# Kernel tuning notes

Hardware: AMD Instinct MI355X
Metric: run time of the kernel (lower is better)

## Reference

```python
import jax, jax.numpy as jnp
import numpy as np

N_NODES = 50000
N_EDGES = 800000
IN_C, HID_C, OUT_C = 128, 256, 64


def _linear_params(key, fan_in, fan_out):
    kw, kb = jax.random.split(key)
    bound = 1.0 / np.sqrt(fan_in)
    w = jax.random.uniform(kw, (fan_in, fan_out), jnp.float32, -bound, bound)
    b = jax.random.uniform(kb, (fan_out,), jnp.float32, -bound, bound)
    return w, b


def setup_inputs() -> dict:
    key = jax.random.key(0)
    ks = jax.random.split(key, 8)
    x = jax.random.normal(ks[0], (N_NODES, IN_C), jnp.float32)
    edge_index = jax.random.randint(ks[1], (2, N_EDGES), 0, N_NODES, dtype=jnp.int64)
    w1a, b1a = _linear_params(ks[2], IN_C, HID_C)
    w1b, b1b = _linear_params(ks[3], HID_C, HID_C)
    w2a, b2a = _linear_params(ks[4], HID_C, HID_C)
    w2b, b2b = _linear_params(ks[5], HID_C, HID_C)
    w3a, b3a = _linear_params(ks[6], HID_C, HID_C)
    w3b, b3b = _linear_params(ks[7], HID_C, OUT_C)
    return {
        "x": x, "edge_index": edge_index,
        "w1a": w1a, "b1a": b1a, "w1b": w1b, "b1b": b1b,
        "w2a": w2a, "b2a": b2a, "w2b": w2b, "b2b": b2b,
        "w3a": w3a, "b3a": b3a, "w3b": w3b, "b3b": b3b,
    }


def _gin_conv(x, src, dst, wa, ba, wb, bb):
    # GINConv (eps=0): MLP( x + sum_{j->i} x_j )
    agg = jax.ops.segment_sum(x[src], dst, num_segments=N_NODES)  # [N, d]
    h = x + agg
    h = jnp.maximum(h @ wa + ba, 0.0)
    return h @ wb + bb


def reference(x, edge_index, w1a, b1a, w1b, b1b, w2a, b2a, w2b, b2b,
              w3a, b3a, w3b, b3b):
    src, dst = edge_index[0], edge_index[1]
    h = jnp.maximum(_gin_conv(x, src, dst, w1a, b1a, w1b, b1b), 0.0)
    h = jnp.maximum(_gin_conv(h, src, dst, w2a, b2a, w2b, b2b), 0.0)
    # output head: Linear -> ReLU -> Dropout(eval: identity) -> Linear
    h = jnp.maximum(h @ w3a + b3a, 0.0)
    return h @ w3b + b3b  # [N, OUT_C]
```

## Files before the change

### kernel.cpp

```cpp
#include <hip/hip_runtime.h>
#include <stdint.h>

#define N_NODES 50000
#define N_EDGES 800000
#define M_PAD   50048
#define NREP    4
#define MCAP    8
#define SCAP    24
#define BCAP    (MCAP + SCAP)
#define CSTR    50048
#define NPX     6256
#define TSTR    264

typedef __attribute__((ext_vector_type(8))) short bf16x8;
typedef __attribute__((ext_vector_type(4))) float f32x4;

__device__ __forceinline__ unsigned short f2b(float f){
    unsigned int u = __builtin_bit_cast(unsigned int, f);
    u += 0x7fffu + ((u >> 16) & 1u);
    return (unsigned short)(u >> 16);
}
__device__ __forceinline__ float b2f(unsigned short s){
    unsigned int u = ((unsigned int)s) << 16;
    return __builtin_bit_cast(float, u);
}

__device__ __forceinline__ void gl_lds16(const void* g, void* l){
    __builtin_amdgcn_global_load_lds(
        (const __attribute__((address_space(1))) void*)g,
        (__attribute__((address_space(3))) void*)l, 16, 0, 0);
}

__global__ void k_x2b(const float* __restrict__ x, unsigned short* __restrict__ xs,
                      int* __restrict__ cnt){
    int gi = blockIdx.x * 256 + threadIdx.x;
    if (gi < NREP * CSTR) cnt[gi] = 0;
    size_t e0 = (size_t)gi * 8;
    if (e0 >= (size_t)M_PAD * 128) return;
    int node = (int)(e0 >> 7);
    int ch0  = (int)(e0 & 127);
    int sl = ch0 >> 5, wth = ch0 & 31;
    bf16x8 o;
    if (node < N_NODES){
        const float4* xp = (const float4*)(x + e0);
        float4 a = xp[0], b = xp[1];
        o[0] = (short)f2b(a.x); o[1] = (short)f2b(a.y);
        o[2] = (short)f2b(a.z); o[3] = (short)f2b(a.w);
        o[4] = (short)f2b(b.x); o[5] = (short)f2b(b.y);
        o[6] = (short)f2b(b.z); o[7] = (short)f2b(b.w);
    } else {
#pragma unroll
        for (int i = 0; i < 8; ++i) o[i] = 0;
    }
    *(bf16x8*)&xs[((size_t)(sl * 50048 + node)) * 32 + wth] = o;
}

__global__ __launch_bounds__(256) void k_scatter(const int* __restrict__ ei,
        int* __restrict__ cnt, unsigned short* __restrict__ mn,
        unsigned short* __restrict__ sp){
    const int x = blockIdx.x & 7;
    const int c = blockIdx.x >> 3;
    const int nlo = x * NPX, nhi = nlo + NPX;
    const int r = threadIdx.x & 3;
#pragma unroll
    for (int i = 0; i < 4; ++i){
        int e = c * 1024 + i * 256 + threadIdx.x;
        if (e < N_EDGES){
            int d = ei[N_EDGES + e];
            if (d >= nlo && d < nhi && (unsigned)d < N_NODES){
                unsigned s = (unsigned)ei[e];
                if (s < N_NODES){
                    int p = atomicAdd(&cnt[r * CSTR + d], 1);
                    int b = (d << 2) + r;
                    if (p < MCAP) mn[(b << 3) + p] = (unsigned short)s;
                    else if (p < BCAP) sp[b * SCAP + (p - MCAP)] = (unsigned short)s;
                }
            }
        }
    }
}

__global__ void k_scan1(const int* __restrict__ cnt, int* __restrict__ bsum){
    __shared__ int s[256];
    int t = threadIdx.x, n = blockIdx.x * 256 + t;
    int v = 0;
    if (n < M_PAD){
#pragma unroll
        for (int r = 0; r < 4; ++r){
            int c = cnt[r * CSTR + n];
            v += (c > BCAP) ? BCAP : c;
        }
        v = (v + 3) & ~3;
    }
    s[t] = v;
    __syncthreads();
    for (int off = 128; off > 0; off >>= 1){
        if (t < off) s[t] += s[t + off];
        __syncthreads();
    }
    if (t == 0) bsum[blockIdx.x] = s[0];
}

__global__ void k_scan2(const int* __restrict__ bsum, int* __restrict__ boff){
    __shared__ int s[256];
    int t = threadIdx.x;
    int v = (t < 196) ? bsum[t] : 0;
    s[t] = v;
    __syncthreads();
    for (int off = 1; off < 256; off <<= 1){
        int a = (t >= off) ? s[t - off] : 0;
        __syncthreads();
        s[t] += a;
        __syncthreads();
    }
    boff[t] = s[t] - v;
}

__global__ void k_scan3(const int* __restrict__ cnt, const int* __restrict__ boff,
                        int* __restrict__ mgoff){
    __shared__ int s[256];
    int t = threadIdx.x, n = blockIdx.x * 256 + t;
    int v = 0;
    if (n < M_PAD){
#pragma unroll
        for (int r = 0; r < 4; ++r){
            int c = cnt[r * CSTR + n];
            v += (c > BCAP) ? BCAP : c;
        }
        v = (v + 3) & ~3;
    }
    s[t] = v;
    __syncthreads();
    for (int off = 1; off < 256; off <<= 1){
        int a = (t >= off) ? s[t - off] : 0;
        __syncthreads();
        s[t] += a;
        __syncthreads();
    }
    if (n < M_PAD) mgoff[n] = boff[blockIdx.x] + s[t] - v;
}

__global__ void k_merge(const int* __restrict__ cnt, const int* __restrict__ mgoff,
                        const unsigned short* __restrict__ mn, const unsigned short* __restrict__ sp,
                        unsigned short* __restrict__ mg, int* __restrict__ mginfo){
    const int t = threadIdx.x;
    const int r = t & 3;
    const int n = blockIdx.x * 64 + (t >> 2);
    int c = cnt[r * CSTR + n];
    if (c > BCAP) c = BCAP;
    int incl = c;
    int t1 = __shfl_up(incl, 1, 4); if (r >= 1) incl += t1;
    int t2 = __shfl_up(incl, 2, 4); if (r >= 2) incl += t2;
    const int excl = incl - c;
    const int total = __shfl(incl, 3, 4);
    const unsigned mb = (unsigned)mgoff[n];
    const unsigned short* src = &mn[((n << 2) + r) << 3];
    for (int i = 0; i < c && i < MCAP; ++i)
        mg[mb + excl + i] = src[i];
    const unsigned short* ssrc = &sp[((n << 2) + r) * SCAP];
    for (int i = MCAP; i < c; ++i)
        mg[mb + excl + i] = ssrc[i - MCAP];
    if (r == 3){
        int grp = (total + 3) >> 2;
        mginfo[n] = ((int)mb << 6) | grp;
        for (int pos = total; pos < grp * 4; ++pos) mg[mb + pos] = (unsigned short)N_NODES;
    }
}

template<int C, bool SPLIT>
__global__ __launch_bounds__(256) void k_aggx(const unsigned short* __restrict__ in,
        const int* __restrict__ mginfo, const unsigned short* __restrict__ mg,
        unsigned short* __restrict__ out){
    constexpr int RS = C / 8;
    const int bid = blockIdx.x, w8 = bid & 7;
    int g, nbase;
    if (SPLIT){ g = w8 & 3; nbase = ((bid >> 3) + (w8 >> 2) * 391) * 64; }
    else      { g = w8;     nbase = (bid >> 3) * 64; }
    const int lane = threadIdx.x & 63, wid = threadIdx.x >> 6;
    const int qd = lane >> 2, lq = lane & 3;
    const int n = nbase + wid * 16 + qd;
    const bf16x8* __restrict__ xr = (const bf16x8*)in;
    const unsigned sbu = (unsigned)g * 50048u;

    float a[8];
    {
        bf16x8 s = xr[(sbu + (unsigned)n) * 4u + (unsigned)lq];
#pragma unroll
        for (int i = 0; i < 8; ++i) a[i] = b2f((unsigned short)s[i]);
    }
    const int info = mginfo[n];
    const int grp = info & 63;
    const unsigned mbase = (unsigned)(info >> 6);
    for (int k = 0; k < grp; ++k){
        ushort4 jj = *(const ushort4*)&mg[mbase + (unsigned)(k * 4)];
        bf16x8 v0 = xr[(sbu + jj.x) * 4u + lq];
        bf16x8 v1 = xr[(sbu + jj.y) * 4u + lq];
        bf16x8 v2 = xr[(sbu + jj.z) * 4u + lq];
        bf16x8 v3 = xr[(sbu + jj.w) * 4u + lq];
#pragma unroll
        for (int i = 0; i < 8; ++i)
            a[i] += (b2f((unsigned short)v0[i]) + b2f((unsigned short)v1[i]))
                  + (b2f((unsigned short)v2[i]) + b2f((unsigned short)v3[i]));
    }
    bf16x8 o;
#pragma unroll
    for (int i = 0; i < 8; ++i) o[i] = (short)f2b(a[i]);
    *(bf16x8*)&out[((unsigned)n * RS + (unsigned)(g * 4 + lq)) * 8u] = o;
}

__global__ void k_wt_all(const float* w0, const float* w1, const float* w2,
                         const float* w3, const float* w4, const float* w5,
                         unsigned short* o0, unsigned short* o1, unsigned short* o2,
                         unsigned short* o3, unsigned short* o4, unsigned short* o5){
    const int Ks[6]  = {128, 256, 256, 256, 256, 256};
    const int Ns[6]  = {256, 256, 256, 256, 256,  64};
    const int NPs[6] = {256, 256, 256, 256, 256, 128};
    int s = blockIdx.y;
    const float* w = (s == 0) ? w0 : (s == 1) ? w1 : (s == 2) ? w2
                   : (s == 3) ? w3 : (s == 4) ? w4 : w5;
    unsigned short* o = (s == 0) ? o0 : (s == 1) ? o1 : (s == 2) ? o2
                      : (s == 3) ? o3 : (s == 4) ? o4 : o5;
    int K = Ks[s], N = Ns[s], NP = NPs[s];
    int idx = blockIdx.x * 256 + threadIdx.x;
    if (idx >= NP * K) return;
    int np = idx / K, k = idx - np * K;
    float v = (np < N) ? w[(size_t)k * N + np] : 0.f;
    o[idx] = f2b(v);
}

template<int K1, int NMID, int NOUT, bool RELU_OUT, bool BF16OUT, bool SLICED>
__global__ __launch_bounds__(256) void k_mlp2(const unsigned short* __restrict__ A,
        const unsigned short* __restrict__ WA, const float* __restrict__ bA,
        const unsigned short* __restrict__ WB, const float* __restrict__ bB,
        void* __restrict__ out, int mstore){
    constexpr int NFA = NMID / 32;
    constexpr int NFB = NOUT / 32;
    __shared__ alignas(16) unsigned short As[64 * 32];
    __shared__ alignas(16) unsigned short Bs[NMID * 32];
    __shared__ alignas(16) unsigned short T[64 * TSTR];
    const int tid  = threadIdx.x;
    const int lane = tid & 63;
    const int c = lane & 15, qq = lane >> 4;
    const int kk = qq * 8;
    const int row0 = blockIdx.x * 64;
    const int wm = (tid >> 6) >> 1, wn = (tid >> 6) & 1;

    const f32x4 fzero = {0.f, 0.f, 0.f, 0.f};
    const char* Ab = (const char*)A;

    {
        f32x4 acc[NFA][2];
#pragma unroll
        for (int nf = 0; nf < NFA; ++nf){ acc[nf][0] = fzero; acc[nf][1] = fzero; }
        const char* Wb = (const char*)WA;
        for (int kt = 0; kt < K1 / 32; ++kt){
            {
                const int o = tid * 16;
                gl_lds16(Ab + ((size_t)(row0 + (o >> 6)) * K1 + kt * 32) * 2 + (o & 63),
                         (char*)As + o);
            }
#pragma unroll
            for (int ch = 0; ch < NMID / 64; ++ch){
                const int o = ch * 4096 + tid * 16;
                gl_lds16(Wb + ((size_t)(o >> 6) * K1 + kt * 32) * 2 + (o & 63),
                         (char*)Bs + o);
            }
            __syncthreads();
            bf16x8 xf[2];
#pragma unroll
            for (int mf = 0; mf < 2; ++mf)
                xf[mf] = *(const bf16x8*)&As[(wm * 32 + mf * 16 + c) * 32 + kk];
#pragma unroll
            for (int nf = 0; nf < NFA; ++nf){
                bf16x8 wf = *(const bf16x8*)&Bs[((wn * NFA + nf) * 16 + c) * 32 + kk];
#pragma unroll
                for (int mf = 0; mf < 2; ++mf)
                    acc[nf][mf] = __builtin_amdgcn_mfma_f32_16x16x32_bf16(wf, xf[mf], acc[nf][mf], 0, 0, 0);
            }
            __syncthreads();
        }
#pragma unroll
        for (int nf = 0; nf < NFA; ++nf){
            const int nb = wn * (NFA * 16) + nf * 16 + qq * 4;
            const float4 bb = *(const float4*)&bA[nb];
#pragma unroll
            for (int mf = 0; mf < 2; ++mf){
                const int ml = wm * 32 + mf * 16 + c;
                float v0 = fmaxf(acc[nf][mf][0] + bb.x, 0.f);
                float v1 = fmaxf(acc[nf][mf][1] + bb.y, 0.f);
                float v2 = fmaxf(acc[nf][mf][2] + bb.z, 0.f);
                float v3 = fmaxf(acc[nf][mf][3] + bb.w, 0.f);
                uint2 p;
                p.x = (unsigned)f2b(v0) | ((unsigned)f2b(v1) << 16);
                p.y = (unsigned)f2b(v2) | ((unsigned)f2b(v3) << 16);
                *(uint2*)&T[ml * TSTR + nb] = p;
            }
        }
    }
    __syncthreads();

    {
        f32x4 acc[NFB][2];
#pragma unroll
        for (int nf = 0; nf < NFB; ++nf){ acc[nf][0] = fzero; acc[nf][1] = fzero; }
        const char* Wb = (const char*)WB;
        for (int kt = 0; kt < NMID / 32; ++kt){
#pragma unroll
            for (int ch = 0; ch < NOUT / 64; ++ch){
                const int o = ch * 4096 + tid * 16;
                gl_lds16(Wb + ((size_t)(o >> 6) * NMID + kt * 32) * 2 + (o & 63),
                         (char*)Bs + o);
            }
            __syncthreads();
            bf16x8 xf[2];
#pragma unroll
            for (int mf = 0; mf < 2; ++mf)
                xf[mf] = *(const bf16x8*)&T[(wm * 32 + mf * 16 + c) * TSTR + kt * 32 + kk];
#pragma unroll
            for (int nf = 0; nf < NFB; ++nf){
                bf16x8 wf = *(const bf16x8*)&Bs[((wn * NFB + nf) * 16 + c) * 32 + kk];
#pragma unroll
                for (int mf = 0; mf < 2; ++mf)
                    acc[nf][mf] = __builtin_amdgcn_mfma_f32_16x16x32_bf16(wf, xf[mf], acc[nf][mf], 0, 0, 0);
            }
            __syncthreads();
        }
#pragma unroll
        for (int nf = 0; nf < NFB; ++nf){
            const int nb = wn * (NFB * 16) + nf * 16 + qq * 4;
            const float4 bb = *(const float4*)&bB[nb];
#pragma unroll
            for (int mf = 0; mf < 2; ++mf){
                const int m = row0 + wm * 32 + mf * 16 + c;
                if (m < mstore){
                    float v0 = acc[nf][mf][0] + bb.x;
                    float v1 = acc[nf][mf][1] + bb.y;
                    float v2 = acc[nf][mf][2] + bb.z;
                    float v3 = acc[nf][mf][3] + bb.w;
                    if (RELU_OUT){
                        v0 = fmaxf(v0, 0.f); v1 = fmaxf(v1, 0.f);
                        v2 = fmaxf(v2, 0.f); v3 = fmaxf(v3, 0.f);
                    }
                    if (SLICED){
                        uint2 p;
                        p.x = (unsigned)f2b(v0) | ((unsigned)f2b(v1) << 16);
                        p.y = (unsigned)f2b(v2) | ((unsigned)f2b(v3) << 16);
                        if (m >= N_NODES){ p.x = 0; p.y = 0; }
                        *(uint2*)&((unsigned short*)out)[
                            ((size_t)((nb >> 5) * 50048 + m)) * 32 + (nb & 31)] = p;
                    } else if (BF16OUT){
                        uint2 p;
                        p.x = (unsigned)f2b(v0) | ((unsigned)f2b(v1) << 16);
                        p.y = (unsigned)f2b(v2) | ((unsigned)f2b(v3) << 16);
                        *(uint2*)&((unsigned short*)out)[(size_t)m * NOUT + nb] = p;
                    } else {
                        float4 p = make_float4(v0, v1, v2, v3);
                        *(float4*)&((float*)out)[(size_t)m * NOUT + nb] = p;
                    }
                }
            }
        }
    }
}

extern "C" void kernel_launch(void* const* d_in, const int* in_sizes, int n_in,
                              void* d_out, int out_size, void* d_ws, size_t ws_size,
                              hipStream_t stream){
    const float* x   = (const float*)d_in[0];
    const int*   ei  = (const int*)d_in[1];
    const float* w1a = (const float*)d_in[2];
    const float* b1a = (const float*)d_in[3];
    const float* w1b = (const float*)d_in[4];
    const float* b1b = (const float*)d_in[5];
    const float* w2a = (const float*)d_in[6];
    const float* b2a = (const float*)d_in[7];
    const float* w2b = (const float*)d_in[8];
    const float* b2b = (const float*)d_in[9];
    const float* w3a = (const float*)d_in[10];
    const float* b3a = (const float*)d_in[11];
    const float* w3b = (const float*)d_in[12];
    const float* b3b = (const float*)d_in[13];

    char* ws = (char*)d_ws;
    size_t off = 0;
    auto take = [&](size_t bytes) -> char* {
        off = (off + 255) & ~(size_t)255;
        char* p = ws + off;
        off += bytes;
        return p;
    };
    unsigned short* xs1  = (unsigned short*)take((size_t)4 * 50048 * 32 * 2);
    unsigned short* g1   = (unsigned short*)take((size_t)M_PAD * 128 * 2);
    unsigned short* h1s  = (unsigned short*)take((size_t)8 * 50048 * 32 * 2);
    unsigned short* g2   = (unsigned short*)take((size_t)M_PAD * 256 * 2);
    unsigned short* h2   = (unsigned short*)take((size_t)M_PAD * 256 * 2);
    unsigned short* wt1a = (unsigned short*)take(256 * 128 * 2);
    unsigned short* wt1b = (unsigned short*)take(256 * 256 * 2);
    unsigned short* wt2a = (unsigned short*)take(256 * 256 * 2);
    unsigned short* wt2b = (unsigned short*)take(256 * 256 * 2);
    unsigned short* wt3a = (unsigned short*)take(256 * 256 * 2);
    unsigned short* wt3b = (unsigned short*)take(128 * 256 * 2);
    int*            cnt  = (int*)take((size_t)NREP * CSTR * 4);
    unsigned short* mn   = (unsigned short*)take((size_t)M_PAD * 4 * MCAP * 2);
    unsigned short* sp   = (unsigned short*)take((size_t)M_PAD * 4 * SCAP * 2);
    unsigned short* mg   = (unsigned short*)take((size_t)1100000 * 2);
    int*            mgoff  = (int*)take((size_t)M_PAD * 4);
    int*            mginfo = (int*)take((size_t)M_PAD * 4);
    int*            bsum = (int*)take(256 * 4);
    int*            boff = (int*)take(256 * 4);

    k_x2b<<<(M_PAD * 128 / 8 + 255) / 256, 256, 0, stream>>>(x, xs1, cnt);
    k_scatter<<<782 * 8, 256, 0, stream>>>(ei, cnt, mn, sp);
    k_scan1<<<196, 256, 0, stream>>>(cnt, bsum);
    k_scan2<<<1,   256, 0, stream>>>(bsum, boff);
    k_scan3<<<196, 256, 0, stream>>>(cnt, boff, mgoff);
    k_merge<<<782, 256, 0, stream>>>(cnt, mgoff, mn, sp, mg, mginfo);
    k_wt_all<<<dim3(256, 6), 256, 0, stream>>>(w1a, w1b, w2a, w2b, w3a, w3b,
                                               wt1a, wt1b, wt2a, wt2b, wt3a, wt3b);

    k_aggx<128, true ><<<391 * 8, 256, 0, stream>>>(xs1, mginfo, mg, g1);
    k_mlp2<128, 256, 256, true, true, true><<<M_PAD / 64, 256, 0, stream>>>(
        g1, wt1a, b1a, wt1b, b1b, h1s, M_PAD);
    k_aggx<256, false><<<782 * 8, 256, 0, stream>>>(h1s, mginfo, mg, g2);
    k_mlp2<256, 256, 256, true, true, false><<<M_PAD / 64, 256, 0, stream>>>(
        g2, wt2a, b2a, wt2b, b2b, h2, M_PAD);
    k_mlp2<256, 256, 64, false, false, false><<<M_PAD / 64, 256, 0, stream>>>(
        h2, wt3a, b3a, wt3b, b3b, d_out, N_NODES);
}
```

Before: 217.9 us.

## Sort nodes by degree bucket for aggregation and sort neighbor lists

Adds a degree histogram and counting sort that builds a node permutation grouping nodes of equal padded degree, so each aggregation wavefront processes nodes with similar neighbor counts and suffers less loop divergence. The scan kernels are restructured to compute the histogram and the per-bin offsets. The merge step now insertion-sorts each replica's neighbor list by source index, which should give more local gather addresses. In exchange it adds an extra indirection through perm, atomics in the scans, and per-thread sorting in merge. Output rows still land at their original node index.

```diff
diff --git a/kernel.cpp b/kernel.cpp
--- a/kernel.cpp
+++ b/kernel.cpp
@@ -10,6 +10,7 @@
 #define BCAP    (MCAP + SCAP)
 #define CSTR    50048
 #define NPX     6256
+#define BINS    33
 #define TSTR    264
 
 typedef __attribute__((ext_vector_type(8))) short bf16x8;
@@ -31,10 +32,21 @@
         (__attribute__((address_space(3))) void*)l, 16, 0, 0);
 }
 
+__device__ __forceinline__ int pdeg(const int* __restrict__ cnt, int n){
+    int v = 0;
+#pragma unroll
+    for (int r = 0; r < 4; ++r){
+        int c = cnt[r * CSTR + n];
+        v += (c > BCAP) ? BCAP : c;
+    }
+    return (v + 3) & ~3;
+}
+
 __global__ void k_x2b(const float* __restrict__ x, unsigned short* __restrict__ xs,
-                      int* __restrict__ cnt){
+                      int* __restrict__ cnt, int* __restrict__ ghist){
     int gi = blockIdx.x * 256 + threadIdx.x;
     if (gi < NREP * CSTR) cnt[gi] = 0;
+    if (gi < BINS) ghist[gi] = 0;
     size_t e0 = (size_t)gi * 8;
     if (e0 >= (size_t)M_PAD * 128) return;
     int node = (int)(e0 >> 7);
@@ -80,28 +92,27 @@
     }
 }
 
-__global__ void k_scan1(const int* __restrict__ cnt, int* __restrict__ bsum){
+__global__ void k_scanA(const int* __restrict__ cnt, int* __restrict__ bsum,
+                        int* __restrict__ ghist){
     __shared__ int s[256];
+    __shared__ int h[BINS];
     int t = threadIdx.x, n = blockIdx.x * 256 + t;
-    int v = 0;
-    if (n < M_PAD){
-#pragma unroll
-        for (int r = 0; r < 4; ++r){
-            int c = cnt[r * CSTR + n];
-            v += (c > BCAP) ? BCAP : c;
-        }
-        v = (v + 3) & ~3;
-    }
+    if (t < BINS) h[t] = 0;
+    int v = (n < M_PAD) ? pdeg(cnt, n) : 0;
     s[t] = v;
+    __syncthreads();
+    if (n < M_PAD) atomicAdd(&h[v >> 2], 1);
     __syncthreads();
     for (int off = 128; off > 0; off >>= 1){
         if (t < off) s[t] += s[t + off];
         __syncthreads();
     }
     if (t == 0) bsum[blockIdx.x] = s[0];
-}
-
-__global__ void k_scan2(const int* __restrict__ bsum, int* __restrict__ boff){
+    if (t < BINS && h[t] > 0) atomicAdd(&ghist[t], h[t]);
+}
+
+__global__ void k_scanB(const int* __restrict__ bsum, int* __restrict__ boff,
+                        const int* __restrict__ ghist, int* __restrict__ bincur){
     __shared__ int s[256];
     int t = threadIdx.x;
     int v = (t < 196) ? bsum[t] : 0;
@@ -113,23 +124,10 @@
         s[t] += a;
         __syncthreads();
     }
-    boff[t] = s[t] - v;
-}
-
-__global__ void k_scan3(const int* __restrict__ cnt, const int* __restrict__ boff,
-                        int* __restrict__ mgoff){
-    __shared__ int s[256];
-    int t = threadIdx.x, n = blockIdx.x * 256 + t;
-    int v = 0;
-    if (n < M_PAD){
-#pragma unroll
-        for (int r = 0; r < 4; ++r){
-            int c = cnt[r * CSTR + n];
-            v += (c > BCAP) ? BCAP : c;
-        }
-        v = (v + 3) & ~3;
-    }
-    s[t] = v;
+    if (t < 196) boff[t] = s[t] - v;
+    __syncthreads();
+    int w = (t < BINS) ? ghist[t] : 0;
+    s[t] = w;
     __syncthreads();
     for (int off = 1; off < 256; off <<= 1){
         int a = (t >= off) ? s[t - off] : 0;
@@ -137,7 +135,35 @@
         s[t] += a;
         __syncthreads();
     }
-    if (n < M_PAD) mgoff[n] = boff[blockIdx.x] + s[t] - v;
+    if (t < BINS) bincur[t] = s[t] - w;
+}
+
+__global__ void k_scanC(const int* __restrict__ cnt, const int* __restrict__ boff,
+                        int* __restrict__ mgoff, int* __restrict__ bincur,
+                        unsigned short* __restrict__ perm){
+    __shared__ int s[256];
+    __shared__ int h[BINS];
+    __shared__ int hb[BINS];
+    int t = threadIdx.x, n = blockIdx.x * 256 + t;
+    int v = (n < M_PAD) ? pdeg(cnt, n) : 0;
+    int grp = v >> 2;
+    s[t] = v;
+    if (t < BINS) h[t] = 0;
+    __syncthreads();
+    int lpos = 0;
+    if (n < M_PAD) lpos = atomicAdd(&h[grp], 1);
+    __syncthreads();
+    if (t < BINS && h[t] > 0) hb[t] = atomicAdd(&bincur[t], h[t]);
+    for (int off = 1; off < 256; off <<= 1){
+        int a = (t >= off) ? s[t - off] : 0;
+        __syncthreads();
+        s[t] += a;
+        __syncthreads();
+    }
+    if (n < M_PAD){
+        mgoff[n] = boff[blockIdx.x] + s[t] - v;
+        perm[hb[grp] + lpos] = (unsigned short)n;
+    }
 }
 
 __global__ void k_merge(const int* __restrict__ cnt, const int* __restrict__ mgoff,
@@ -148,18 +174,25 @@
     const int n = blockIdx.x * 64 + (t >> 2);
     int c = cnt[r * CSTR + n];
     if (c > BCAP) c = BCAP;
+    unsigned short v[BCAP];
+    const unsigned short* src = &mn[((n << 2) + r) << 3];
+    for (int i = 0; i < c && i < MCAP; ++i) v[i] = src[i];
+    const unsigned short* ssrc = &sp[((n << 2) + r) * SCAP];
+    for (int i = MCAP; i < c; ++i) v[i] = ssrc[i - MCAP];
+    for (int i = 1; i < c; ++i){
+        unsigned short key = v[i];
+        int j = i - 1;
+        while (j >= 0 && v[j] > key){ v[j + 1] = v[j]; --j; }
+        v[j + 1] = key;
+    }
     int incl = c;
     int t1 = __shfl_up(incl, 1, 4); if (r >= 1) incl += t1;
     int t2 = __shfl_up(incl, 2, 4); if (r >= 2) incl += t2;
     const int excl = incl - c;
     const int total = __shfl(incl, 3, 4);
     const unsigned mb = (unsigned)mgoff[n];
-    const unsigned short* src = &mn[((n << 2) + r) << 3];
-    for (int i = 0; i < c && i < MCAP; ++i)
-        mg[mb + excl + i] = src[i];
-    const unsigned short* ssrc = &sp[((n << 2) + r) * SCAP];
-    for (int i = MCAP; i < c; ++i)
-        mg[mb + excl + i] = ssrc[i - MCAP];
+    for (int i = 0; i < c; ++i)
+        mg[mb + excl + i] = v[i];
     if (r == 3){
         int grp = (total + 3) >> 2;
         mginfo[n] = ((int)mb << 6) | grp;
@@ -170,15 +203,15 @@
 template<int C, bool SPLIT>
 __global__ __launch_bounds__(256) void k_aggx(const unsigned short* __restrict__ in,
         const int* __restrict__ mginfo, const unsigned short* __restrict__ mg,
-        unsigned short* __restrict__ out){
+        const unsigned short* __restrict__ perm, unsigned short* __restrict__ out){
     constexpr int RS = C / 8;
     const int bid = blockIdx.x, w8 = bid & 7;
-    int g, nbase;
-    if (SPLIT){ g = w8 & 3; nbase = ((bid >> 3) + (w8 >> 2) * 391) * 64; }
-    else      { g = w8;     nbase = (bid >> 3) * 64; }
+    int g, pbase;
+    if (SPLIT){ g = w8 & 3; pbase = ((bid >> 3) + (w8 >> 2) * 391) * 64; }
+    else      { g = w8;     pbase = (bid >> 3) * 64; }
     const int lane = threadIdx.x & 63, wid = threadIdx.x >> 6;
     const int qd = lane >> 2, lq = lane & 3;
-    const int n = nbase + wid * 16 + qd;
+    const int n = perm[pbase + wid * 16 + qd];
     const bf16x8* __restrict__ xr = (const bf16x8*)in;
     const unsigned sbu = (unsigned)g * 50048u;
 
@@ -408,20 +441,23 @@
     int*            mginfo = (int*)take((size_t)M_PAD * 4);
     int*            bsum = (int*)take(256 * 4);
     int*            boff = (int*)take(256 * 4);
-
-    k_x2b<<<(M_PAD * 128 / 8 + 255) / 256, 256, 0, stream>>>(x, xs1, cnt);
+    int*            ghist  = (int*)take(BINS * 4);
+    int*            bincur = (int*)take(BINS * 4);
+    unsigned short* perm   = (unsigned short*)take((size_t)M_PAD * 2);
+
+    k_x2b<<<(M_PAD * 128 / 8 + 255) / 256, 256, 0, stream>>>(x, xs1, cnt, ghist);
     k_scatter<<<782 * 8, 256, 0, stream>>>(ei, cnt, mn, sp);
-    k_scan1<<<196, 256, 0, stream>>>(cnt, bsum);
-    k_scan2<<<1,   256, 0, stream>>>(bsum, boff);
-    k_scan3<<<196, 256, 0, stream>>>(cnt, boff, mgoff);
+    k_scanA<<<196, 256, 0, stream>>>(cnt, bsum, ghist);
+    k_scanB<<<1,   256, 0, stream>>>(bsum, boff, ghist, bincur);
+    k_scanC<<<196, 256, 0, stream>>>(cnt, boff, mgoff, bincur, perm);
     k_merge<<<782, 256, 0, stream>>>(cnt, mgoff, mn, sp, mg, mginfo);
     k_wt_all<<<dim3(256, 6), 256, 0, stream>>>(w1a, w1b, w2a, w2b, w3a, w3b,
                                                wt1a, wt1b, wt2a, wt2b, wt3a, wt3b);
 
-    k_aggx<128, true ><<<391 * 8, 256, 0, stream>>>(xs1, mginfo, mg, g1);
+    k_aggx<128, true ><<<391 * 8, 256, 0, stream>>>(xs1, mginfo, mg, perm, g1);
     k_mlp2<128, 256, 256, true, true, true><<<M_PAD / 64, 256, 0, stream>>>(
         g1, wt1a, b1a, wt1b, b1b, h1s, M_PAD);
-    k_aggx<256, false><<<782 * 8, 256, 0, stream>>>(h1s, mginfo, mg, g2);
+    k_aggx<256, false><<<782 * 8, 256, 0, stream>>>(h1s, mginfo, mg, perm, g2);
     k_mlp2<256, 256, 256, true, true, false><<<M_PAD / 64, 256, 0, stream>>>(
         g2, wt2a, b2a, wt2b, b2b, h2, M_PAD);
     k_mlp2<256, 256, 64, false, false, false><<<M_PAD / 64, 256, 0, stream>>>(
```

New measurement: 359.9 us. 65.2% more time.

## Sort neighbor lists per bucket and unpack bf16 pairs via 32-bit masks

Applied to the files above, without the earlier changes.

In the merge kernel, each per-replica neighbor bucket (up to 32 entries) is loaded into registers and sorted with a bitonic network before being written to the merged list. Sorted source indices should make the gathers in the aggregation kernel more cache- and TLB-friendly. The aggregation kernel now loads rows as 4x32-bit words and unpacks bf16 pairs with a shift and a mask instead of per-element 16-bit extraction, which should cut conversion ALU work. The sort adds register pressure and compare-swap work to the merge kernel, and it changes the order of the float summation.

```diff
diff --git a/kernel.cpp b/kernel.cpp
--- a/kernel.cpp
+++ b/kernel.cpp
@@ -14,6 +14,7 @@
 
 typedef __attribute__((ext_vector_type(8))) short bf16x8;
 typedef __attribute__((ext_vector_type(4))) float f32x4;
+typedef __attribute__((ext_vector_type(4))) unsigned int u32x4;
 
 __device__ __forceinline__ unsigned short f2b(float f){
     unsigned int u = __builtin_bit_cast(unsigned int, f);
@@ -24,11 +25,24 @@
     unsigned int u = ((unsigned int)s) << 16;
     return __builtin_bit_cast(float, u);
 }
+__device__ __forceinline__ float bcf(unsigned int u){
+    return __builtin_bit_cast(float, u);
+}
 
 __device__ __forceinline__ void gl_lds16(const void* g, void* l){
     __builtin_amdgcn_global_load_lds(
         (const __attribute__((address_space(1))) void*)g,
         (__attribute__((address_space(3))) void*)l, 16, 0, 0);
+}
+
+__device__ __forceinline__ int pdeg(const int* __restrict__ cnt, int n){
+    int v = 0;
+#pragma unroll
+    for (int r = 0; r < 4; ++r){
+        int c = cnt[r * CSTR + n];
+        v += (c > BCAP) ? BCAP : c;
+    }
+    return (v + 3) & ~3;
 }
 
 __global__ void k_x2b(const float* __restrict__ x, unsigned short* __restrict__ xs,
@@ -83,15 +97,7 @@
 __global__ void k_scan1(const int* __restrict__ cnt, int* __restrict__ bsum){
     __shared__ int s[256];
     int t = threadIdx.x, n = blockIdx.x * 256 + t;
-    int v = 0;
-    if (n < M_PAD){
-#pragma unroll
-        for (int r = 0; r < 4; ++r){
-            int c = cnt[r * CSTR + n];
-            v += (c > BCAP) ? BCAP : c;
-        }
-        v = (v + 3) & ~3;
-    }
+    int v = (n < M_PAD) ? pdeg(cnt, n) : 0;
     s[t] = v;
     __syncthreads();
     for (int off = 128; off > 0; off >>= 1){
@@ -120,15 +126,7 @@
                         int* __restrict__ mgoff){
     __shared__ int s[256];
     int t = threadIdx.x, n = blockIdx.x * 256 + t;
-    int v = 0;
-    if (n < M_PAD){
-#pragma unroll
-        for (int r = 0; r < 4; ++r){
-            int c = cnt[r * CSTR + n];
-            v += (c > BCAP) ? BCAP : c;
-        }
-        v = (v + 3) & ~3;
-    }
+    int v = (n < M_PAD) ? pdeg(cnt, n) : 0;
     s[t] = v;
     __syncthreads();
     for (int off = 1; off < 256; off <<= 1){
@@ -148,18 +146,53 @@
     const int n = blockIdx.x * 64 + (t >> 2);
     int c = cnt[r * CSTR + n];
     if (c > BCAP) c = BCAP;
+
+    const unsigned short* src  = &mn[((n << 2) + r) << 3];
+    const unsigned short* ssrc = &sp[((n << 2) + r) * SCAP];
+    unsigned short v[BCAP];
+    {
+        ushort4 m0 = *(const ushort4*)(src);
+        ushort4 m1 = *(const ushort4*)(src + 4);
+        v[0]=m0.x; v[1]=m0.y; v[2]=m0.z; v[3]=m0.w;
+        v[4]=m1.x; v[5]=m1.y; v[6]=m1.z; v[7]=m1.w;
+#pragma unroll
+        for (int q = 0; q < 6; ++q){
+            ushort4 sq = *(const ushort4*)(ssrc + q * 4);
+            v[8 + q*4 + 0] = sq.x; v[8 + q*4 + 1] = sq.y;
+            v[8 + q*4 + 2] = sq.z; v[8 + q*4 + 3] = sq.w;
+        }
+    }
+#pragma unroll
+    for (int i = 0; i < BCAP; ++i)
+        if (i >= c) v[i] = 0xFFFFu;
+
+#pragma unroll
+    for (int k = 2; k <= 32; k <<= 1){
+#pragma unroll
+        for (int j = k >> 1; j > 0; j >>= 1){
+#pragma unroll
+            for (int i = 0; i < 32; ++i){
+                const int l = i ^ j;
+                if (l > i){
+                    const bool up = ((i & k) == 0);
+                    unsigned short a = v[i], b = v[l];
+                    bool sw = up ? (a > b) : (a < b);
+                    unsigned short lo = sw ? b : a, hi = sw ? a : b;
+                    v[i] = lo; v[l] = hi;
+                }
+            }
+        }
+    }
+
     int incl = c;
     int t1 = __shfl_up(incl, 1, 4); if (r >= 1) incl += t1;
     int t2 = __shfl_up(incl, 2, 4); if (r >= 2) incl += t2;
     const int excl = incl - c;
     const int total = __shfl(incl, 3, 4);
     const unsigned mb = (unsigned)mgoff[n];
-    const unsigned short* src = &mn[((n << 2) + r) << 3];
-    for (int i = 0; i < c && i < MCAP; ++i)
-        mg[mb + excl + i] = src[i];
-    const unsigned short* ssrc = &sp[((n << 2) + r) * SCAP];
-    for (int i = MCAP; i < c; ++i)
-        mg[mb + excl + i] = ssrc[i - MCAP];
+#pragma unroll
+    for (int i = 0; i < BCAP; ++i)
+        if (i < c) mg[mb + excl + i] = v[i];
     if (r == 3){
         int grp = (total + 3) >> 2;
         mginfo[n] = ((int)mb << 6) | grp;
@@ -179,32 +212,41 @@
     const int lane = threadIdx.x & 63, wid = threadIdx.x >> 6;
     const int qd = lane >> 2, lq = lane & 3;
     const int n = nbase + wid * 16 + qd;
-    const bf16x8* __restrict__ xr = (const bf16x8*)in;
+    const u32x4* __restrict__ xr = (const u32x4*)in;
     const unsigned sbu = (unsigned)g * 50048u;
 
-    float a[8];
+    float alo[4], ahi[4];
     {
-        bf16x8 s = xr[(sbu + (unsigned)n) * 4u + (unsigned)lq];
-#pragma unroll
-        for (int i = 0; i < 8; ++i) a[i] = b2f((unsigned short)s[i]);
+        u32x4 s = xr[(sbu + (unsigned)n) * 4u + (unsigned)lq];
+#pragma unroll
+        for (int j = 0; j < 4; ++j){
+            alo[j] = bcf(s[j] << 16);
+            ahi[j] = bcf(s[j] & 0xFFFF0000u);
+        }
     }
     const int info = mginfo[n];
     const int grp = info & 63;
     const unsigned mbase = (unsigned)(info >> 6);
     for (int k = 0; k < grp; ++k){
         ushort4 jj = *(const ushort4*)&mg[mbase + (unsigned)(k * 4)];
-        bf16x8 v0 = xr[(sbu + jj.x) * 4u + lq];
-        bf16x8 v1 = xr[(sbu + jj.y) * 4u + lq];
-        bf16x8 v2 = xr[(sbu + jj.z) * 4u + lq];
-        bf16x8 v3 = xr[(sbu + jj.w) * 4u + lq];
-#pragma unroll
-        for (int i = 0; i < 8; ++i)
-            a[i] += (b2f((unsigned short)v0[i]) + b2f((unsigned short)v1[i]))
-                  + (b2f((unsigned short)v2[i]) + b2f((unsigned short)v3[i]));
+        u32x4 v0 = xr[(sbu + jj.x) * 4u + lq];
+        u32x4 v1 = xr[(sbu + jj.y) * 4u + lq];
+        u32x4 v2 = xr[(sbu + jj.z) * 4u + lq];
+        u32x4 v3 = xr[(sbu + jj.w) * 4u + lq];
+#pragma unroll
+        for (int j = 0; j < 4; ++j){
+            alo[j] += (bcf(v0[j] << 16) + bcf(v1[j] << 16))
+                    + (bcf(v2[j] << 16) + bcf(v3[j] << 16));
+            ahi[j] += (bcf(v0[j] & 0xFFFF0000u) + bcf(v1[j] & 0xFFFF0000u))
+                    + (bcf(v2[j] & 0xFFFF0000u) + bcf(v3[j] & 0xFFFF0000u));
+        }
     }
     bf16x8 o;
 #pragma unroll
-    for (int i = 0; i < 8; ++i) o[i] = (short)f2b(a[i]);
+    for (int j = 0; j < 4; ++j){
+        o[2*j]     = (short)f2b(alo[j]);
+        o[2*j + 1] = (short)f2b(ahi[j]);
+    }
     *(bf16x8*)&out[((unsigned)n * RS + (unsigned)(g * 4 + lq)) * 8u] = o;
 }
 
```

Result: no change. 219.8 us (+0.9%).
